# Kernel optimization log

Hardware: AMD Instinct MI355X
Metric: run time of the kernel (lower is better)

Reference implementation:

```python
import jax, jax.numpy as jnp
import numpy as np

B, T, NOBJ = 512, 20, 36
D, V, EMB, E = 2048, 10000, 300, 512
HM, HO = 1024, 256


def setup_inputs() -> dict:
    key = jax.random.key(0)
    ks = jax.random.split(key, 20)
    s = 0.05
    return {
        "obj_enc": jax.random.normal(ks[0], (B, NOBJ, D), jnp.float32),
        "x": jax.random.randint(ks[1], (B, T), 0, V, dtype=jnp.int32),
        "q_means_mask": jax.random.normal(ks[2], (B, T, E), jnp.float32),
        "q_logs_mask": jax.random.normal(ks[3], (B, T, E), jnp.float32) * 0.1,
        "q_z_mask": jax.random.normal(ks[4], (B, T, E), jnp.float32),
        "q_means_obj": jax.random.normal(ks[5], (B, T, E), jnp.float32),
        "q_logs_obj": jax.random.normal(ks[6], (B, T, E), jnp.float32) * 0.1,
        "q_z_obj": jax.random.normal(ks[7], (B, T, E), jnp.float32),
        # learned parameters
        "emd_W": jax.random.normal(ks[8], (V, EMB), jnp.float32) * s,
        "W_ih_m": jax.random.normal(ks[9], (4 * HM, D + E + EMB), jnp.float32) * s,
        "W_hh_m": jax.random.normal(ks[10], (4 * HM, HM), jnp.float32) * s,
        "b_m": jax.random.normal(ks[11], (4 * HM,), jnp.float32) * s,
        "W_ih_o": jax.random.normal(ks[12], (4 * HO, D + 2 * E + EMB), jnp.float32) * s,
        "W_hh_o": jax.random.normal(ks[13], (4 * HO, HO), jnp.float32) * s,
        "b_o": jax.random.normal(ks[14], (4 * HO,), jnp.float32) * s,
        "fc_m_W": jax.random.normal(ks[15], (2 * E, HM), jnp.float32) * s,
        "fc_m_b": jax.random.normal(ks[16], (2 * E,), jnp.float32) * s,
        "fc_o_W": jax.random.normal(ks[17], (2 * E, HO), jnp.float32) * s,
        "fc_o_b": jax.random.normal(ks[18], (2 * E,), jnp.float32) * s,
    }


def _lstm_cell(xt, h, c, W_ih, W_hh, b):
    # torch LSTMCell gate order: i, f, g, o
    g = xt @ W_ih.T + h @ W_hh.T + b
    i, f, gg, o = jnp.split(g, 4, axis=-1)
    c = jax.nn.sigmoid(f) * c + jax.nn.sigmoid(i) * jnp.tanh(gg)
    h = jax.nn.sigmoid(o) * jnp.tanh(c)
    return h, c


def _kl(p_means, p_logs, q_means, q_logs):
    return (0.5 * (p_logs - q_logs)
            + (jnp.exp(q_logs) + (q_means - p_means) ** 2) / (2.0 * jnp.exp(p_logs))
            - 0.5)


def reference(obj_enc, x, q_means_mask, q_logs_mask, q_z_mask,
              q_means_obj, q_logs_obj, q_z_obj,
              emd_W, W_ih_m, W_hh_m, b_m, W_ih_o, W_hh_o, b_o,
              fc_m_W, fc_m_b, fc_o_W, fc_o_b):
    bsz = obj_enc.shape[0]
    # masked mean over object regions
    obj_mask = (jnp.sum(jnp.abs(obj_enc), axis=-1) > 0).astype(obj_enc.dtype)  # [B,N]
    meanimfeats = (obj_enc * obj_mask[..., None]).sum(1) / jnp.maximum(obj_mask.sum(1, keepdims=True), 1e-9)  # [B,D]

    seq_mask = ((x != 0) & (x != 2)).astype(jnp.float32)  # [B,T]
    x_emb = emd_W[x]  # [B,T,EMB]

    # teacher-forced previous latents (zeros at t=0)
    z_m_prev = jnp.concatenate([jnp.zeros_like(q_z_mask[:, :1]), q_z_mask[:, :-1]], axis=1)
    z_o_prev = jnp.concatenate([jnp.zeros_like(q_z_obj[:, :1]), q_z_obj[:, :-1]], axis=1)

    xs = (jnp.swapaxes(x_emb, 0, 1), jnp.swapaxes(z_m_prev, 0, 1),
          jnp.swapaxes(q_z_mask, 0, 1), jnp.swapaxes(z_o_prev, 0, 1))  # time-major

    init = (jnp.zeros((bsz, HM), obj_enc.dtype), jnp.zeros((bsz, HM), obj_enc.dtype),
            jnp.zeros((bsz, HO), obj_enc.dtype), jnp.zeros((bsz, HO), obj_enc.dtype))

    def step(carry, ins):
        h_m, c_m, h_o, c_o = carry
        xt, zmp, zmc, zop = ins
        h_m, c_m = _lstm_cell(jnp.concatenate([zmp, xt, meanimfeats], -1), h_m, c_m, W_ih_m, W_hh_m, b_m)
        out_m = h_m @ fc_m_W.T + fc_m_b  # [B,2E]
        h_o, c_o = _lstm_cell(jnp.concatenate([zmc, zop, xt, meanimfeats], -1), h_o, c_o, W_ih_o, W_hh_o, b_o)
        out_o = h_o @ fc_o_W.T + fc_o_b  # [B,2E]
        return (h_m, c_m, h_o, c_o), (out_m, out_o)

    _, (outs_m, outs_o) = jax.lax.scan(step, init, xs)  # [T,B,2E]
    outs_m = jnp.swapaxes(outs_m, 0, 1)  # [B,T,2E]
    outs_o = jnp.swapaxes(outs_o, 0, 1)

    p_means_mask, p_logs_mask = outs_m[..., :E], outs_m[..., E:]
    p_means_obj, p_logs_obj = outs_o[..., :E], outs_o[..., E:]

    kl_mask = (_kl(p_means_mask, p_logs_mask, q_means_mask, q_logs_mask).sum(-1) * seq_mask).sum(-1)
    kl_obj = (_kl(p_means_obj, p_logs_obj, q_means_obj, q_logs_obj).sum(-1) * seq_mask).sum(-1)
    return kl_mask + kl_obj  # [B]
```

## Files before the change

### kernel.cpp

```cpp
#include <hip/hip_runtime.h>

#define Bz 512
#define Tz 20
#define NOBJz 36
#define Dz 2048
#define EMBz 300
#define Ez 512
#define HMz 1024
#define HOz 256
#define KXM 832
#define KXO 1344

typedef short v8s __attribute__((ext_vector_type(8)));
typedef float v4f __attribute__((ext_vector_type(4)));
typedef unsigned short u16;

__device__ __forceinline__ float sigf(float x) { return 1.f / (1.f + __expf(-x)); }
__device__ __forceinline__ float tanhfast(float x) { return 2.f * sigf(2.f * x) - 1.f; }

__device__ __forceinline__ u16 f2bf(float f) {
    union { float f; unsigned u; } v; v.f = f;
    unsigned u = v.u;
    u += 0x7FFFu + ((u >> 16) & 1u);
    return (u16)(u >> 16);
}
__device__ __forceinline__ float bf2f(u16 h) {
    union { unsigned u; float f; } v; v.u = ((unsigned)h) << 16;
    return v.f;
}


__global__ void obj_mask_kernel(const float* __restrict__ obj_enc, float* __restrict__ mask) {
    int bn = blockIdx.x, lane = threadIdx.x;
    const float* row = obj_enc + (size_t)bn * Dz;
    float s = 0.f;
    for (int d = lane; d < Dz; d += 64) s += fabsf(row[d]);
    for (int off = 32; off > 0; off >>= 1) s += __shfl_down(s, off);
    if (lane == 0) mask[bn] = (s > 0.f) ? 1.f : 0.f;
}

__global__ void meanim_kernel(const float* __restrict__ obj_enc, const float* __restrict__ mask,
                              u16* __restrict__ meanim_bf) {
    int idx = blockIdx.x * 256 + threadIdx.x;
    if (idx >= Bz * Dz) return;
    int b = idx / Dz, d = idx - b * Dz;
    float s = 0.f, cnt = 0.f;
    for (int n = 0; n < NOBJz; ++n) {
        float m = mask[b * NOBJz + n];
        cnt += m;
        s += obj_enc[((size_t)b * NOBJz + n) * Dz + d] * m;
    }
    meanim_bf[idx] = f2bf(s / fmaxf(cnt, 1e-9f));
}

__global__ void convert_pad(u16* __restrict__ dst, const float* __restrict__ src,
                            int rows, int src_cols, int ld_src, int col0, int dst_ld, int permH) {
    int idx = blockIdx.x * 256 + threadIdx.x;
    if (idx >= rows * dst_ld) return;
    int rp = idx / dst_ld, c = idx - rp * dst_ld;
    int n = rp;
    if (permH) { int g = (rp >> 4) & 3, u = (rp >> 6) * 16 + (rp & 15); n = g * permH + u; }
    dst[idx] = (c < src_cols) ? f2bf(src[(size_t)n * ld_src + col0 + c]) : (u16)0;
}

__global__ void bias_perm(float* __restrict__ dst, const float* __restrict__ src, int H) {
    int r = blockIdx.x * 256 + threadIdx.x;
    if (r >= 4 * H) return;
    int g = (r >> 4) & 3, u = (r >> 6) * 16 + (r & 15);
    dst[r] = src[g * H + u];
}

__global__ void assemble_Xm(u16* __restrict__ X, const float* __restrict__ qzm,
                            const int* __restrict__ x, const float* __restrict__ emd) {
    int idx = blockIdx.x * 256 + threadIdx.x;
    if (idx >= Tz * Bz * KXM) return;
    int r = idx / KXM, c = idx - r * KXM;
    int t = r / Bz, b = r - t * Bz;
    float v;
    if (c < Ez)             v = (t > 0) ? qzm[((size_t)b * Tz + (t - 1)) * Ez + c] : 0.f;
    else if (c < Ez + EMBz) { int xv = x[b * Tz + t]; v = emd[(size_t)xv * EMBz + (c - Ez)]; }
    else                    v = 0.f;
    X[idx] = f2bf(v);
}

__global__ void assemble_Xo(u16* __restrict__ X, const float* __restrict__ qzm,
                            const float* __restrict__ qzo, const int* __restrict__ x,
                            const float* __restrict__ emd) {
    int idx = blockIdx.x * 256 + threadIdx.x;
    if (idx >= Tz * Bz * KXO) return;
    int r = idx / KXO, c = idx - r * KXO;
    int t = r / Bz, b = r - t * Bz;
    float v;
    if (c < Ez)                 v = qzm[((size_t)b * Tz + t) * Ez + c];
    else if (c < 2 * Ez)        v = (t > 0) ? qzo[((size_t)b * Tz + (t - 1)) * Ez + (c - Ez)] : 0.f;
    else if (c < 2 * Ez + EMBz) { int xv = x[b * Tz + t]; v = emd[(size_t)xv * EMBz + (c - 2 * Ez)]; }
    else                        v = 0.f;
    X[idx] = f2bf(v);
}


__device__ __forceinline__ void mma128(
    const u16* __restrict__ A, int lda, const u16* __restrict__ W, int ldw, int K,
    int bm, int bn, u16* As, u16* Ws, v4f (&acc)[4][4]) {
    const int tid = threadIdx.x;
    const int lane = tid & 63, w = tid >> 6;
    const int wm = w >> 1, wn = w & 1;
    const int r15 = lane & 15, quad = lane >> 4;
    const int lrow = lane >> 3;
    const int lcol = ((lane & 7) ^ lrow) * 8;
    for (int k0 = 0; k0 < K; k0 += 64) {
        const u16* gA = A + (size_t)bm * lda + k0;
        const u16* gW = W + (size_t)bn * ldw + k0;
#pragma unroll
        for (int c = 0; c < 4; ++c) {
            int chunk = w * 4 + c;
            int row = chunk * 8 + lrow;
            __builtin_amdgcn_global_load_lds(
                (const __attribute__((address_space(1))) unsigned int*)(gA + (size_t)row * lda + lcol),
                (__attribute__((address_space(3))) unsigned int*)(As + chunk * 512), 16, 0, 0);
            __builtin_amdgcn_global_load_lds(
                (const __attribute__((address_space(1))) unsigned int*)(gW + (size_t)row * ldw + lcol),
                (__attribute__((address_space(3))) unsigned int*)(Ws + chunk * 512), 16, 0, 0);
        }
        __syncthreads();
#pragma unroll
        for (int kk = 0; kk < 64; kk += 32) {
            v8s a[4], b[4];
#pragma unroll
            for (int i = 0; i < 4; ++i) {
                int r = wm * 64 + 16 * i + r15;
                a[i] = *(const v8s*)&As[r * 64 + (((kk >> 3) + quad) ^ (r15 & 7)) * 8];
            }
#pragma unroll
            for (int j = 0; j < 4; ++j) {
                int r = wn * 64 + 16 * j + r15;
                b[j] = *(const v8s*)&Ws[r * 64 + (((kk >> 3) + quad) ^ (r15 & 7)) * 8];
            }
#pragma unroll
            for (int i = 0; i < 4; ++i)
#pragma unroll
                for (int j = 0; j < 4; ++j)
                    acc[i][j] = __builtin_amdgcn_mfma_f32_16x16x32_bf16(a[i], b[j], acc[i][j], 0, 0, 0);
        }
        __syncthreads();
    }
}

__global__ __launch_bounds__(256) void gemm128(
    const u16* __restrict__ A, int lda, const u16* __restrict__ W, int ldw,
    void* __restrict__ Cv, int ldc, int K,
    const float* __restrict__ bias, const u16* __restrict__ addR, unsigned addR_mask, int out_bf16) {
    __shared__ u16 As[128 * 64];
    __shared__ u16 Ws[128 * 64];
    v4f acc[4][4] = {};
    const int bm = blockIdx.y * 128, bn = blockIdx.x * 128;
    mma128(A, lda, W, ldw, K, bm, bn, As, Ws, acc);
    const int tid = threadIdx.x, lane = tid & 63, w = tid >> 6;
    const int wm = w >> 1, wn = w & 1, r15 = lane & 15, quad = lane >> 4;
    float* Cf = (float*)Cv;
    u16* Cb = (u16*)Cv;
#pragma unroll
    for (int i = 0; i < 4; ++i)
#pragma unroll
        for (int j = 0; j < 4; ++j) {
            int col = bn + wn * 64 + 16 * j + r15;
            float bv = bias ? bias[col] : 0.f;
#pragma unroll
            for (int r = 0; r < 4; ++r) {
                int row = bm + wm * 64 + 16 * i + quad * 4 + r;
                float v = acc[i][j][r] + bv;
                if (addR) v += bf2f(addR[(size_t)(row & addR_mask) * ldc + col]);
                if (out_bf16) Cb[(size_t)row * ldc + col] = f2bf(v);
                else          Cf[(size_t)row * ldc + col] = v;
            }
        }
}

__global__ __launch_bounds__(256) void step_fused(
    const u16* __restrict__ Hm_prev, const u16* __restrict__ Whh_m, const u16* __restrict__ Gm,
    float* __restrict__ cm, u16* __restrict__ hm,
    const u16* __restrict__ Ho_prev, const u16* __restrict__ Whh_o, const u16* __restrict__ Go,
    float* __restrict__ co, u16* __restrict__ ho) {
    __shared__ u16 As[128 * 64];
    __shared__ u16 Ws[128 * 64];
    v4f acc[4][4] = {};
    const int bx = blockIdx.x;
    const u16 *A, *W, *G;
    float* c;
    u16* h;
    int lda, N4, H, bm, bn, K;
    if (bx < 128) {
        bm = (bx >> 5) * 128; bn = (bx & 31) * 128;
        A = Hm_prev; W = Whh_m; G = Gm; c = cm; h = hm; lda = HMz; N4 = 4 * HMz; H = HMz; K = HMz;
    } else {
        int lx = bx - 128;
        bm = (lx >> 3) * 128; bn = (lx & 7) * 128;
        A = Ho_prev; W = Whh_o; G = Go; c = co; h = ho; lda = HOz; N4 = 4 * HOz; H = HOz; K = HOz;
    }
    mma128(A, lda, W, lda, K, bm, bn, As, Ws, acc);
    const int tid = threadIdx.x, lane = tid & 63, w = tid >> 6;
    const int wm = w >> 1, wn = w & 1, r15 = lane & 15, quad = lane >> 4;
    const int u = ((bn + wn * 64) >> 6) * 16 + r15;
#pragma unroll
    for (int i = 0; i < 4; ++i)
#pragma unroll
        for (int r = 0; r < 4; ++r) {
            int b = bm + wm * 64 + 16 * i + quad * 4 + r;
            size_t gb = (size_t)b * N4 + bn + wn * 64 + r15;
            float gi = acc[i][0][r] + bf2f(G[gb]);
            float gf = acc[i][1][r] + bf2f(G[gb + 16]);
            float gg = acc[i][2][r] + bf2f(G[gb + 32]);
            float go = acc[i][3][r] + bf2f(G[gb + 48]);
            size_t ci = (size_t)b * H + u;
            float cn = sigf(gf) * c[ci] + sigf(gi) * tanhfast(gg);
            c[ci] = cn;
            h[ci] = f2bf(sigf(go) * tanhfast(cn));
        }
}

__global__ void cell0(const u16* __restrict__ Gm, float* __restrict__ cm, u16* __restrict__ hm,
                      const u16* __restrict__ Go, float* __restrict__ co, u16* __restrict__ ho) {
    int idx = blockIdx.x * 256 + threadIdx.x;
    if (idx < Bz * HMz) {
        int b = idx / HMz, u = idx - b * HMz;
        size_t gb = (size_t)b * 4 * HMz + ((u >> 4) * 64 + (u & 15));
        float gi = bf2f(Gm[gb]), gf = bf2f(Gm[gb + 16]), gg = bf2f(Gm[gb + 32]), go = bf2f(Gm[gb + 48]);
        (void)gf;
        float cn = sigf(gi) * tanhfast(gg);
        cm[idx] = cn;
        hm[idx] = f2bf(sigf(go) * tanhfast(cn));
    } else {
        idx -= Bz * HMz;
        if (idx >= Bz * HOz) return;
        int b = idx / HOz, u = idx - b * HOz;
        size_t gb = (size_t)b * 4 * HOz + ((u >> 4) * 64 + (u & 15));
        float gi = bf2f(Go[gb]), gg = bf2f(Go[gb + 32]), go = bf2f(Go[gb + 48]);
        float cn = sigf(gi) * tanhfast(gg);
        co[idx] = cn;
        ho[idx] = f2bf(sigf(go) * tanhfast(cn));
    }
}

__global__ __launch_bounds__(256) void kl_kernel(
    const float* __restrict__ outs_m, const float* __restrict__ outs_o,
    const float* __restrict__ qmm, const float* __restrict__ qlm,
    const float* __restrict__ qmo, const float* __restrict__ qlo,
    const int* __restrict__ x, float* __restrict__ out) {
    int b = blockIdx.x, tid = threadIdx.x;
    float total = 0.f;
    for (int t = 0; t < Tz; ++t) {
        int xv = x[b * Tz + t];
        if (xv == 0 || xv == 2) continue;
        const float* pm = outs_m + ((size_t)t * Bz + b) * 1024;
        const float* po = outs_o + ((size_t)t * Bz + b) * 1024;
        const size_t q = ((size_t)b * Tz + t) * Ez;
        for (int e = tid; e < Ez; e += 256) {
            float pmm = pm[e], plm = pm[Ez + e];
            float dm = qmm[q + e] - pmm;
            total += 0.5f * (plm - qlm[q + e]) + (__expf(qlm[q + e]) + dm * dm) / (2.f * __expf(plm)) - 0.5f;
            float pmo = po[e], plo = po[Ez + e];
            float dn = qmo[q + e] - pmo;
            total += 0.5f * (plo - qlo[q + e]) + (__expf(qlo[q + e]) + dn * dn) / (2.f * __expf(plo)) - 0.5f;
        }
    }
    __shared__ float red[256];
    red[tid] = total;
    __syncthreads();
    for (int s = 128; s > 0; s >>= 1) {
        if (tid < s) red[tid] += red[tid + s];
        __syncthreads();
    }
    if (tid == 0) out[b] = red[0];
}

extern "C" void kernel_launch(void* const* d_in, const int* in_sizes, int n_in,
                              void* d_out, int out_size, void* d_ws, size_t ws_size,
                              hipStream_t stream) {
    const float* obj_enc = (const float*)d_in[0];
    const int*   x       = (const int*)d_in[1];
    const float* qmm     = (const float*)d_in[2];
    const float* qlm     = (const float*)d_in[3];
    const float* qzm     = (const float*)d_in[4];
    const float* qmo     = (const float*)d_in[5];
    const float* qlo     = (const float*)d_in[6];
    const float* qzo     = (const float*)d_in[7];
    const float* emd     = (const float*)d_in[8];
    const float* W_ih_m  = (const float*)d_in[9];
    const float* W_hh_m  = (const float*)d_in[10];
    const float* b_m     = (const float*)d_in[11];
    const float* W_ih_o  = (const float*)d_in[12];
    const float* W_hh_o  = (const float*)d_in[13];
    const float* b_o     = (const float*)d_in[14];
    const float* fc_m_W  = (const float*)d_in[15];
    const float* fc_m_b  = (const float*)d_in[16];
    const float* fc_o_W  = (const float*)d_in[17];
    const float* fc_o_b  = (const float*)d_in[18];
    float* out = (float*)d_out;

    char* base = (char*)d_ws;
    size_t off = 0;
    auto alloc = [&](size_t bytes) { char* r = base + off; off += (bytes + 255) & ~(size_t)255; return r; };
    float* mask     = (float*)alloc((size_t)Bz * NOBJz * 4);
    u16* meanim_bf  = (u16*)alloc((size_t)Bz * Dz * 2);
    u16* Whh_m_bf   = (u16*)alloc((size_t)4 * HMz * HMz * 2);
    u16* Whh_o_bf   = (u16*)alloc((size_t)4 * HOz * HOz * 2);
    u16* Winp_m_bf  = (u16*)alloc((size_t)4 * HMz * KXM * 2);
    u16* Winp_o_bf  = (u16*)alloc((size_t)4 * HOz * KXO * 2);
    u16* Wmean_m_bf = (u16*)alloc((size_t)4 * HMz * Dz * 2);
    u16* Wmean_o_bf = (u16*)alloc((size_t)4 * HOz * Dz * 2);
    u16* Wfc_m_bf   = (u16*)alloc((size_t)1024 * HMz * 2);
    u16* Wfc_o_bf   = (u16*)alloc((size_t)1024 * HOz * 2);
    float* b_m_p    = (float*)alloc((size_t)4 * HMz * 4);
    float* b_o_p    = (float*)alloc((size_t)4 * HOz * 4);
    u16* Xin_m      = (u16*)alloc((size_t)Tz * Bz * KXM * 2);
    u16* Xin_o      = (u16*)alloc((size_t)Tz * Bz * KXO * 2);
    u16* const_m_bf = (u16*)alloc((size_t)Bz * 4 * HMz * 2);
    u16* const_o_bf = (u16*)alloc((size_t)Bz * 4 * HOz * 2);
    u16* Ginp_m_bf  = (u16*)alloc((size_t)Tz * Bz * 4 * HMz * 2);
    u16* Ginp_o_bf  = (u16*)alloc((size_t)Tz * Bz * 4 * HOz * 2);
    float* c_m      = (float*)alloc((size_t)Bz * HMz * 4);
    float* c_o      = (float*)alloc((size_t)Bz * HOz * 4);
    u16* H_m        = (u16*)alloc((size_t)Tz * Bz * HMz * 2);
    u16* H_o        = (u16*)alloc((size_t)Tz * Bz * HOz * 2);
    float* outs_m = (float*)Ginp_m_bf;
    float* outs_o = outs_m + (size_t)Tz * Bz * 1024;

    const int TB = Tz * Bz;

    obj_mask_kernel<<<Bz * NOBJz, 64, 0, stream>>>(obj_enc, mask);
    meanim_kernel<<<(Bz * Dz + 255) / 256, 256, 0, stream>>>(obj_enc, mask, meanim_bf);
    assemble_Xm<<<(TB * KXM + 255) / 256, 256, 0, stream>>>(Xin_m, qzm, x, emd);
    assemble_Xo<<<(TB * KXO + 255) / 256, 256, 0, stream>>>(Xin_o, qzm, qzo, x, emd);

    convert_pad<<<(4 * HMz * HMz + 255) / 256, 256, 0, stream>>>(Whh_m_bf, W_hh_m, 4 * HMz, HMz, HMz, 0, HMz, HMz);
    convert_pad<<<(4 * HOz * HOz + 255) / 256, 256, 0, stream>>>(Whh_o_bf, W_hh_o, 4 * HOz, HOz, HOz, 0, HOz, HOz);
    convert_pad<<<(4 * HMz * KXM + 255) / 256, 256, 0, stream>>>(Winp_m_bf, W_ih_m, 4 * HMz, Ez + EMBz, 2860, 0, KXM, HMz);
    convert_pad<<<(4 * HOz * KXO + 255) / 256, 256, 0, stream>>>(Winp_o_bf, W_ih_o, 4 * HOz, 2 * Ez + EMBz, 3372, 0, KXO, HOz);
    convert_pad<<<(4 * HMz * Dz + 255) / 256, 256, 0, stream>>>(Wmean_m_bf, W_ih_m, 4 * HMz, Dz, 2860, Ez + EMBz, Dz, HMz);
    convert_pad<<<(4 * HOz * Dz + 255) / 256, 256, 0, stream>>>(Wmean_o_bf, W_ih_o, 4 * HOz, Dz, 3372, 2 * Ez + EMBz, Dz, HOz);
    convert_pad<<<(1024 * HMz + 255) / 256, 256, 0, stream>>>(Wfc_m_bf, fc_m_W, 1024, HMz, HMz, 0, HMz, 0);
    convert_pad<<<(1024 * HOz + 255) / 256, 256, 0, stream>>>(Wfc_o_bf, fc_o_W, 1024, HOz, HOz, 0, HOz, 0);
    bias_perm<<<(4 * HMz + 255) / 256, 256, 0, stream>>>(b_m_p, b_m, HMz);
    bias_perm<<<(4 * HOz + 255) / 256, 256, 0, stream>>>(b_o_p, b_o, HOz);

    gemm128<<<dim3(4 * HMz / 128, Bz / 128), 256, 0, stream>>>(
        meanim_bf, Dz, Wmean_m_bf, Dz, const_m_bf, 4 * HMz, Dz, b_m_p, nullptr, 0u, 1);
    gemm128<<<dim3(4 * HOz / 128, Bz / 128), 256, 0, stream>>>(
        meanim_bf, Dz, Wmean_o_bf, Dz, const_o_bf, 4 * HOz, Dz, b_o_p, nullptr, 0u, 1);

    gemm128<<<dim3(4 * HMz / 128, TB / 128), 256, 0, stream>>>(
        Xin_m, KXM, Winp_m_bf, KXM, Ginp_m_bf, 4 * HMz, KXM, nullptr, const_m_bf, (unsigned)(Bz - 1), 1);
    gemm128<<<dim3(4 * HOz / 128, TB / 128), 256, 0, stream>>>(
        Xin_o, KXO, Winp_o_bf, KXO, Ginp_o_bf, 4 * HOz, KXO, nullptr, const_o_bf, (unsigned)(Bz - 1), 1);

    cell0<<<(Bz * (HMz + HOz) + 255) / 256, 256, 0, stream>>>(
        Ginp_m_bf, c_m, H_m, Ginp_o_bf, c_o, H_o);

    for (int t = 1; t < Tz; ++t) {
        step_fused<<<160, 256, 0, stream>>>(
            H_m + (size_t)(t - 1) * Bz * HMz, Whh_m_bf, Ginp_m_bf + (size_t)t * Bz * 4 * HMz,
            c_m, H_m + (size_t)t * Bz * HMz,
            H_o + (size_t)(t - 1) * Bz * HOz, Whh_o_bf, Ginp_o_bf + (size_t)t * Bz * 4 * HOz,
            c_o, H_o + (size_t)t * Bz * HOz);
    }

    gemm128<<<dim3(1024 / 128, TB / 128), 256, 0, stream>>>(
        H_m, HMz, Wfc_m_bf, HMz, outs_m, 1024, HMz, fc_m_b, nullptr, 0u, 0);
    gemm128<<<dim3(1024 / 128, TB / 128), 256, 0, stream>>>(
        H_o, HOz, Wfc_o_bf, HOz, outs_o, 1024, HOz, fc_o_b, nullptr, 0u, 0);

    kl_kernel<<<Bz, 256, 0, stream>>>(outs_m, outs_o, qmm, qlm, qmo, qlo, x, out);
}
```

Measured before the change: 1.342 ms.

## Replace per-step recurrent launches with a persistent kernel and grid barrier

The cell0 kernel and the 19 per-timestep step_fused launches are replaced by one persistent kernel of 160 blocks. It loops over all timesteps, keeps the cell state in registers instead of global memory, and syncs blocks between steps with an atomic-counter grid barrier. This removes kernel launch gaps and the global c-state reads and writes. The barrier relies on all 160 blocks being co-resident, which holds on a 256-CU device but is not guaranteed by the launch, and it adds a spin-wait on one atomic.

```diff
diff --git a/kernel.cpp b/kernel.cpp
--- a/kernel.cpp
+++ b/kernel.cpp
@@ -10,6 +10,7 @@
 #define HOz 256
 #define KXM 832
 #define KXO 1344
+#define NBLK 160
 
 typedef short v8s __attribute__((ext_vector_type(8)));
 typedef float v4f __attribute__((ext_vector_type(4)));
@@ -176,68 +177,66 @@
         }
 }
 
-__global__ __launch_bounds__(256) void step_fused(
-    const u16* __restrict__ Hm_prev, const u16* __restrict__ Whh_m, const u16* __restrict__ Gm,
-    float* __restrict__ cm, u16* __restrict__ hm,
-    const u16* __restrict__ Ho_prev, const u16* __restrict__ Whh_o, const u16* __restrict__ Go,
-    float* __restrict__ co, u16* __restrict__ ho) {
+__device__ __forceinline__ void grid_barrier(unsigned* cnt, unsigned target) {
+    __syncthreads();
+    if (threadIdx.x == 0) {
+        __threadfence();
+        atomicAdd(cnt, 1u);
+        while (atomicAdd(cnt, 0u) < target) {}
+    }
+    __syncthreads();
+    __threadfence();
+}
+
+__global__ __launch_bounds__(256) void step_persist(
+    u16* __restrict__ H_m, const u16* __restrict__ Whh_m, const u16* __restrict__ Gm,
+    u16* __restrict__ H_o, const u16* __restrict__ Whh_o, const u16* __restrict__ Go,
+    unsigned* __restrict__ barrier_cnt) {
     __shared__ u16 As[128 * 64];
     __shared__ u16 Ws[128 * 64];
-    v4f acc[4][4] = {};
     const int bx = blockIdx.x;
-    const u16 *A, *W, *G;
-    float* c;
-    u16* h;
-    int lda, N4, H, bm, bn, K;
+    u16* Hbase;
+    const u16 *W, *G;
+    int bm, bn, H, K, N4;
     if (bx < 128) {
         bm = (bx >> 5) * 128; bn = (bx & 31) * 128;
-        A = Hm_prev; W = Whh_m; G = Gm; c = cm; h = hm; lda = HMz; N4 = 4 * HMz; H = HMz; K = HMz;
+        Hbase = H_m; W = Whh_m; G = Gm; H = HMz; K = HMz; N4 = 4 * HMz;
     } else {
         int lx = bx - 128;
         bm = (lx >> 3) * 128; bn = (lx & 7) * 128;
-        A = Ho_prev; W = Whh_o; G = Go; c = co; h = ho; lda = HOz; N4 = 4 * HOz; H = HOz; K = HOz;
-    }
-    mma128(A, lda, W, lda, K, bm, bn, As, Ws, acc);
+        Hbase = H_o; W = Whh_o; G = Go; H = HOz; K = HOz; N4 = 4 * HOz;
+    }
     const int tid = threadIdx.x, lane = tid & 63, w = tid >> 6;
     const int wm = w >> 1, wn = w & 1, r15 = lane & 15, quad = lane >> 4;
     const int u = ((bn + wn * 64) >> 6) * 16 + r15;
+    float cst[4][4];
 #pragma unroll
     for (int i = 0; i < 4; ++i)
 #pragma unroll
-        for (int r = 0; r < 4; ++r) {
-            int b = bm + wm * 64 + 16 * i + quad * 4 + r;
-            size_t gb = (size_t)b * N4 + bn + wn * 64 + r15;
-            float gi = acc[i][0][r] + bf2f(G[gb]);
-            float gf = acc[i][1][r] + bf2f(G[gb + 16]);
-            float gg = acc[i][2][r] + bf2f(G[gb + 32]);
-            float go = acc[i][3][r] + bf2f(G[gb + 48]);
-            size_t ci = (size_t)b * H + u;
-            float cn = sigf(gf) * c[ci] + sigf(gi) * tanhfast(gg);
-            c[ci] = cn;
-            h[ci] = f2bf(sigf(go) * tanhfast(cn));
-        }
-}
-
-__global__ void cell0(const u16* __restrict__ Gm, float* __restrict__ cm, u16* __restrict__ hm,
-                      const u16* __restrict__ Go, float* __restrict__ co, u16* __restrict__ ho) {
-    int idx = blockIdx.x * 256 + threadIdx.x;
-    if (idx < Bz * HMz) {
-        int b = idx / HMz, u = idx - b * HMz;
-        size_t gb = (size_t)b * 4 * HMz + ((u >> 4) * 64 + (u & 15));
-        float gi = bf2f(Gm[gb]), gf = bf2f(Gm[gb + 16]), gg = bf2f(Gm[gb + 32]), go = bf2f(Gm[gb + 48]);
-        (void)gf;
-        float cn = sigf(gi) * tanhfast(gg);
-        cm[idx] = cn;
-        hm[idx] = f2bf(sigf(go) * tanhfast(cn));
-    } else {
-        idx -= Bz * HMz;
-        if (idx >= Bz * HOz) return;
-        int b = idx / HOz, u = idx - b * HOz;
-        size_t gb = (size_t)b * 4 * HOz + ((u >> 4) * 64 + (u & 15));
-        float gi = bf2f(Go[gb]), gg = bf2f(Go[gb + 32]), go = bf2f(Go[gb + 48]);
-        float cn = sigf(gi) * tanhfast(gg);
-        co[idx] = cn;
-        ho[idx] = f2bf(sigf(go) * tanhfast(cn));
+        for (int r = 0; r < 4; ++r) cst[i][r] = 0.f;
+
+    for (int t = 0; t < Tz; ++t) {
+        v4f acc[4][4] = {};
+        if (t > 0)
+            mma128(Hbase + (size_t)(t - 1) * Bz * H, H, W, H, K, bm, bn, As, Ws, acc);
+        const u16* Gt = G + (size_t)t * Bz * N4;
+        u16* Ht = Hbase + (size_t)t * Bz * H;
+#pragma unroll
+        for (int i = 0; i < 4; ++i)
+#pragma unroll
+            for (int r = 0; r < 4; ++r) {
+                int b = bm + wm * 64 + 16 * i + quad * 4 + r;
+                size_t gb = (size_t)b * N4 + bn + wn * 64 + r15;
+                float gi = acc[i][0][r] + bf2f(Gt[gb]);
+                float gf = acc[i][1][r] + bf2f(Gt[gb + 16]);
+                float gg = acc[i][2][r] + bf2f(Gt[gb + 32]);
+                float go = acc[i][3][r] + bf2f(Gt[gb + 48]);
+                float cn = sigf(gf) * cst[i][r] + sigf(gi) * tanhfast(gg);
+                cst[i][r] = cn;
+                Ht[(size_t)b * H + u] = f2bf(sigf(go) * tanhfast(cn));
+            }
+        if (t < Tz - 1)
+            grid_barrier(barrier_cnt, (unsigned)NBLK * (unsigned)(t + 1));
     }
 }
 
@@ -312,20 +311,21 @@
     u16* Wfc_o_bf   = (u16*)alloc((size_t)1024 * HOz * 2);
     float* b_m_p    = (float*)alloc((size_t)4 * HMz * 4);
     float* b_o_p    = (float*)alloc((size_t)4 * HOz * 4);
+    unsigned* bar   = (unsigned*)alloc(256);
     u16* Xin_m      = (u16*)alloc((size_t)Tz * Bz * KXM * 2);
     u16* Xin_o      = (u16*)alloc((size_t)Tz * Bz * KXO * 2);
     u16* const_m_bf = (u16*)alloc((size_t)Bz * 4 * HMz * 2);
     u16* const_o_bf = (u16*)alloc((size_t)Bz * 4 * HOz * 2);
     u16* Ginp_m_bf  = (u16*)alloc((size_t)Tz * Bz * 4 * HMz * 2);
     u16* Ginp_o_bf  = (u16*)alloc((size_t)Tz * Bz * 4 * HOz * 2);
-    float* c_m      = (float*)alloc((size_t)Bz * HMz * 4);
-    float* c_o      = (float*)alloc((size_t)Bz * HOz * 4);
     u16* H_m        = (u16*)alloc((size_t)Tz * Bz * HMz * 2);
     u16* H_o        = (u16*)alloc((size_t)Tz * Bz * HOz * 2);
     float* outs_m = (float*)Ginp_m_bf;
     float* outs_o = outs_m + (size_t)Tz * Bz * 1024;
 
     const int TB = Tz * Bz;
+
+    hipMemsetAsync(bar, 0, 256, stream);
 
     obj_mask_kernel<<<Bz * NOBJz, 64, 0, stream>>>(obj_enc, mask);
     meanim_kernel<<<(Bz * Dz + 255) / 256, 256, 0, stream>>>(obj_enc, mask, meanim_bf);
@@ -353,16 +353,8 @@
     gemm128<<<dim3(4 * HOz / 128, TB / 128), 256, 0, stream>>>(
         Xin_o, KXO, Winp_o_bf, KXO, Ginp_o_bf, 4 * HOz, KXO, nullptr, const_o_bf, (unsigned)(Bz - 1), 1);
 
-    cell0<<<(Bz * (HMz + HOz) + 255) / 256, 256, 0, stream>>>(
-        Ginp_m_bf, c_m, H_m, Ginp_o_bf, c_o, H_o);
-
-    for (int t = 1; t < Tz; ++t) {
-        step_fused<<<160, 256, 0, stream>>>(
-            H_m + (size_t)(t - 1) * Bz * HMz, Whh_m_bf, Ginp_m_bf + (size_t)t * Bz * 4 * HMz,
-            c_m, H_m + (size_t)t * Bz * HMz,
-            H_o + (size_t)(t - 1) * Bz * HOz, Whh_o_bf, Ginp_o_bf + (size_t)t * Bz * 4 * HOz,
-            c_o, H_o + (size_t)t * Bz * HOz);
-    }
+    step_persist<<<NBLK, 256, 0, stream>>>(
+        H_m, Whh_m_bf, Ginp_m_bf, H_o, Whh_o_bf, Ginp_o_bf, bar);
 
     gemm128<<<dim3(1024 / 128, TB / 128), 256, 0, stream>>>(
         H_m, HMz, Wfc_m_bf, HMz, outs_m, 1024, HMz, fc_m_b, nullptr, 0u, 0);
```

Measured after the change: 1.624 ms. 1.21x slower.
